# Performance work log

Hardware: AMD Instinct MI355X
Metric: run time of the kernel (lower is better)

The kernel has to match this reference:

```python
import jax, jax.numpy as jnp
import numpy as np

NB_HEAD = 16
SIZE_PER_HEAD = 64
D_MODEL = NB_HEAD * SIZE_PER_HEAD  # 1024
B, S = 4, 2048
NEG_BIG = 1e10


def setup_inputs() -> dict:
    key = jax.random.key(0)
    ks = jax.random.split(key, 9)
    glorot = lambda k, shape: jax.random.uniform(
        k, shape, jnp.float32, -1.0, 1.0) * np.sqrt(6.0 / (shape[0] + shape[1]))
    return {
        "Q_emb": jax.random.normal(ks[0], (B, S, D_MODEL), jnp.float32),
        "K_emb": jax.random.normal(ks[1], (B, S, D_MODEL), jnp.float32),
        "V_emb": jax.random.normal(ks[2], (B, S, D_MODEL), jnp.float32),
        "Q_ini": jax.random.randint(ks[3], (B, S), 0, 50),
        "K_ini": jax.random.randint(ks[4], (B, S), 0, 50),
        "WQ": glorot(ks[5], (D_MODEL, D_MODEL)),
        "WK": glorot(ks[6], (D_MODEL, D_MODEL)),
        "WV": glorot(ks[7], (D_MODEL, D_MODEL)),
        "WO": glorot(ks[8], (D_MODEL, D_MODEL)),
    }


def _proj(x, W):
    # [B,S,D] @ [D, H*dh] -> [B,H,S,dh]
    b, s, _ = x.shape
    y = jnp.einsum('bsd,de->bse', x, W)
    return y.reshape(b, s, NB_HEAD, SIZE_PER_HEAD).transpose(0, 2, 1, 3)


def reference(Q_emb, K_emb, V_emb, Q_ini, K_ini, WQ, WK, WV, WO):
    b, sq, _ = Q_emb.shape
    sk = K_emb.shape[1]
    q = _proj(Q_emb, WQ)
    k = _proj(K_emb, WK)
    v = _proj(V_emb, WV)
    scores = jnp.einsum('bhqd,bhkd->bhqk', q, k) / jnp.sqrt(
        jnp.asarray(SIZE_PER_HEAD, scores_dtype := q.dtype))
    # pad mask: 1 where key token id != 0, broadcast over queries
    pad = (K_ini != 0).astype(scores.dtype)[:, None, None, :]  # [B,1,1,Sk]
    # sub mask: cumsum of eye along rows == lower-triangular causal mask
    causal = jnp.tril(jnp.ones((sq, sk), scores.dtype))[None, None]  # [1,1,Sq,Sk]
    mask = jnp.minimum(pad, causal)
    scores = scores - (1.0 - mask) * NEG_BIG
    attn = jax.nn.softmax(scores, axis=-1)
    ctx = jnp.einsum('bhqk,bhkd->bhqd', attn, v)
    ctx = ctx.transpose(0, 2, 1, 3).reshape(b, sq, NB_HEAD * SIZE_PER_HEAD)
    return jnp.einsum('bsd,de->bse', ctx, WO)
```

## Files before the change

### kernel.cpp

```cpp
#include <hip/hip_runtime.h>

typedef __bf16 bf16_t;
typedef __bf16 bf16x8 __attribute__((ext_vector_type(8)));
typedef __bf16 bf16x4 __attribute__((ext_vector_type(4)));
typedef float  f32x4  __attribute__((ext_vector_type(4)));

#define S_LEN 2048
#define NH    16
#define DH    64
#define DM    1024
#define BATCH 4
#define LOG2E 1.44269504088896f
#define NEGB  (-1.44269504e10f)

static __device__ __forceinline__ f32x4 mfma16(bf16x8 a, bf16x8 b, f32x4 c) {
    return __builtin_amdgcn_mfma_f32_16x16x32_bf16(a, b, c, 0, 0, 0);
}

#if __has_builtin(__builtin_amdgcn_exp2f)
static __device__ __forceinline__ float exp2_hw(float x) {
    return __builtin_amdgcn_exp2f(x);
}
#else
static __device__ __forceinline__ float exp2_hw(float x) {
    float r;
    asm("v_exp_f32 %0, %1" : "=v"(r) : "v"(x));
    return r;
}
#endif

static __device__ __forceinline__ void gl_lds16(const bf16_t* g, bf16_t* l) {
    __builtin_amdgcn_global_load_lds(
        (const __attribute__((address_space(1))) unsigned int*)g,
        (__attribute__((address_space(3))) unsigned int*)l, 16, 0, 0);
}

__global__ __launch_bounds__(256) void cvt3_bf16(const float* __restrict__ s0,
                                                 const float* __restrict__ s1,
                                                 const float* __restrict__ s2,
                                                 bf16_t* __restrict__ d0,
                                                 bf16_t* __restrict__ d1,
                                                 bf16_t* __restrict__ d2, int n) {
    int z = blockIdx.y;
    const float* s = (z == 0) ? s0 : (z == 1) ? s1 : s2;
    bf16_t*      d = (z == 0) ? d0 : (z == 1) ? d1 : d2;
    int i = (blockIdx.x * 256 + threadIdx.x) * 8;
    if (i >= n) return;
    const float4* q = (const float4*)(s + i);
    float4 a = q[0], b = q[1];
    bf16x8 r;
    r[0] = (bf16_t)a.x; r[1] = (bf16_t)a.y; r[2] = (bf16_t)a.z; r[3] = (bf16_t)a.w;
    r[4] = (bf16_t)b.x; r[5] = (bf16_t)b.y; r[6] = (bf16_t)b.z; r[7] = (bf16_t)b.w;
    *(bf16x8*)(d + i) = r;
}

__global__ __launch_bounds__(256) void wtrans(const float* __restrict__ W,
                                              bf16_t* __restrict__ Wt, float scale) {
    __shared__ bf16_t tile[32][33];
    int x = threadIdx.x, ty = threadIdx.y;
    int bx = blockIdx.x * 32, by = blockIdx.y * 32;
#pragma unroll
    for (int i = 0; i < 4; ++i) {
        int y = ty * 4 + i;
        tile[y][x] = (bf16_t)(W[(by + y) * DM + bx + x] * scale);
    }
    __syncthreads();
#pragma unroll
    for (int i = 0; i < 4; ++i) {
        int y = ty * 4 + i;
        Wt[(bx + y) * DM + by + x] = tile[x][y];
    }
}

template <typename CT>
__global__ __launch_bounds__(512) void gemm_nt_256(const bf16_t* __restrict__ A,
                                                   const bf16_t* __restrict__ Bt,
                                                   CT* __restrict__ C,
                                                   int M, int N, int K, float alpha,
                                                   size_t zsA, size_t zsB, size_t zsC,
                                                   int tz, int ldct) {
    __shared__ __align__(16) bf16_t As[2 * 256 * 32];
    __shared__ __align__(16) bf16_t Bs[2 * 128 * 32];
    A  += (size_t)blockIdx.z * zsA;
    Bt += (size_t)blockIdx.z * zsB;
    C  += (size_t)blockIdx.z * zsC;
    int tid = threadIdx.x, wave = tid >> 6, lane = tid & 63;
    int l15 = lane & 15, quad = lane >> 4;
    int wm = wave >> 1, wn = wave & 1;
    int bm = blockIdx.x * 256, bn = blockIdx.y * 128;
    int srow = lane >> 2, skx = (lane & 3) << 3;

    f32x4 acc[4][4] = {};

    for (int k0 = 0; k0 < K; k0 += 64) {
#pragma unroll
        for (int c = 0; c < 4; ++c) {
            int t = wave * 4 + c;
            int kk = t & 1, rb = (t >> 1) * 16;
            gl_lds16(A + (size_t)(bm + rb + srow) * K + k0 + kk * 32 + skx,
                     As + kk * 8192 + rb * 32);
        }
#pragma unroll
        for (int c = 0; c < 2; ++c) {
            int t = wave * 2 + c;
            int kk = t & 1, rb = (t >> 1) * 16;
            gl_lds16(Bt + (size_t)(bn + rb + srow) * K + k0 + kk * 32 + skx,
                     Bs + kk * 4096 + rb * 32);
        }
        __syncthreads();

#pragma unroll
        for (int kk = 0; kk < 2; ++kk) {
            bf16x8 af[4], bfr[4];
#pragma unroll
            for (int i = 0; i < 4; ++i)
                af[i] = *(const bf16x8*)(As + kk * 8192 +
                                         (wm * 64 + i * 16 + l15) * 32 + quad * 8);
#pragma unroll
            for (int j = 0; j < 4; ++j)
                bfr[j] = *(const bf16x8*)(Bs + kk * 4096 +
                                          (wn * 64 + j * 16 + l15) * 32 + quad * 8);
#pragma unroll
            for (int i = 0; i < 4; ++i)
#pragma unroll
                for (int j = 0; j < 4; ++j)
                    acc[i][j] = mfma16(af[i], bfr[j], acc[i][j]);
        }
        __syncthreads();
    }

    if ((int)blockIdx.z == tz) {
#pragma unroll
        for (int i = 0; i < 4; ++i)
#pragma unroll
            for (int j = 0; j < 4; ++j) {
                int n = bn + wn * 64 + j * 16 + l15;
                int m = bm + wm * 64 + i * 16 + quad * 4;
                bf16x4 c;
#pragma unroll
                for (int r = 0; r < 4; ++r) c[r] = (bf16_t)(acc[i][j][r] * alpha);
                *(bf16x4*)((bf16_t*)C + (size_t)n * ldct + m) = c;
            }
    } else {
#pragma unroll
        for (int i = 0; i < 4; ++i)
#pragma unroll
            for (int r = 0; r < 4; ++r) {
                int row = bm + wm * 64 + i * 16 + quad * 4 + r;
#pragma unroll
                for (int j = 0; j < 4; ++j)
                    C[(size_t)row * N + bn + wn * 64 + j * 16 + l15] =
                        (CT)(acc[i][j][r] * alpha);
            }
    }
}

__global__ __launch_bounds__(256) void vmean_vt(const bf16_t* __restrict__ VT,
                                                float* __restrict__ Vm, int ldv) {
    __shared__ float red[64][4];
    int z = blockIdx.y;
    int row = blockIdx.x * 64 + (threadIdx.x >> 2);
    int part = threadIdx.x & 3;
    const bf16_t* p = VT + (size_t)row * ldv + (size_t)z * S_LEN + part * 512;
    float s = 0.f;
    for (int i = 0; i < 64; ++i) {
        bf16x8 v = *(const bf16x8*)(p + i * 8);
#pragma unroll
        for (int j = 0; j < 8; ++j) s += (float)v[j];
    }
    red[threadIdx.x >> 2][part] = s;
    __syncthreads();
    if (threadIdx.x < 64) {
        float t = red[threadIdx.x][0] + red[threadIdx.x][1] +
                  red[threadIdx.x][2] + red[threadIdx.x][3];
        Vm[z * DM + blockIdx.x * 64 + threadIdx.x] = t * (1.0f / S_LEN);
    }
}

__global__ __launch_bounds__(256) void attn_kernel(const bf16_t* __restrict__ Qp,
                                                   const bf16_t* __restrict__ Kp,
                                                   const bf16_t* __restrict__ VT,
                                                   const int* __restrict__ Kini,
                                                   const float* __restrict__ Vmean,
                                                   bf16_t* __restrict__ ctx,
                                                   int ldv, int nqt) {
    __shared__ __align__(16) bf16_t Ks[64 * 72];
    __shared__ __align__(16) bf16_t VsT[64 * 72];
    __shared__ __align__(16) bf16_t Ps[4][16 * 72];
    __shared__ bf16_t padb[2048];

    int bid = blockIdx.x;
    int qt = nqt - 1 - (bid >> 6);
    int hz = bid & 63;
    int h = hz & 15, z = hz >> 4;
    int tid = threadIdx.x, wave = tid >> 6, lane = tid & 63;
    int l15 = lane & 15, quad = lane >> 4;
    int qbase = qt * 64 + wave * 16;
    size_t rowz = (size_t)z * S_LEN;
    int ntiles = qt + 1;
    int nkeys = ntiles * 64;

    for (int i = tid; i < nkeys; i += 256)
        padb[i] = (Kini[rowz + i] == 0) ? (bf16_t)NEGB : (bf16_t)(0.0f);

    const bf16_t* qptr = Qp + (rowz + qbase + l15) * DM + h * DH + quad * 8;
    bf16x8 qa0 = *(const bf16x8*)qptr;
    bf16x8 qa1 = *(const bf16x8*)(qptr + 32);

    f32x4 o[4] = {};
    f32x4 l4 = {0.f, 0.f, 0.f, 0.f};
    int q = qbase + l15;

    int srow = tid >> 2, sch = (tid & 3) << 4;
    const bf16_t* kgb = Kp + (rowz + srow) * DM + h * DH + sch;
    const bf16_t* vgb = VT + (size_t)(h * DH + srow) * ldv + rowz + sch;

    bf16x8 kr0 = *(const bf16x8*)kgb,        kr1 = *(const bf16x8*)(kgb + 8);
    bf16x8 vr0 = *(const bf16x8*)vgb,        vr1 = *(const bf16x8*)(vgb + 8);

    for (int kt = 0; kt < ntiles; ++kt) {
        int kb = kt * 64;
        *(bf16x8*)(Ks  + srow * 72 + sch)     = kr0;
        *(bf16x8*)(Ks  + srow * 72 + sch + 8) = kr1;
        *(bf16x8*)(VsT + srow * 72 + sch)     = vr0;
        *(bf16x8*)(VsT + srow * 72 + sch + 8) = vr1;
        __syncthreads();

        int nkb = (kt + 1 < ntiles) ? kb + 64 : kb;
        const bf16_t* kg = kgb + (size_t)nkb * DM;
        const bf16_t* vg = vgb + nkb;
        kr0 = *(const bf16x8*)kg; kr1 = *(const bf16x8*)(kg + 8);
        vr0 = *(const bf16x8*)vg; vr1 = *(const bf16x8*)(vg + 8);

        f32x4 sv[4];
#pragma unroll
        for (int ks = 0; ks < 4; ++ks) {
            bf16x8 kf0 = *(const bf16x8*)(Ks + (ks * 16 + l15) * 72 + quad * 8);
            bf16x8 kf1 = *(const bf16x8*)(Ks + (ks * 16 + l15) * 72 + 32 + quad * 8);
            f32x4 s = {0.f, 0.f, 0.f, 0.f};
            s = mfma16(kf0, qa0, s);
            s = mfma16(kf1, qa1, s);
            bf16x4 pb = *(const bf16x4*)(padb + kb + ks * 16 + quad * 4);
#pragma unroll
            for (int r = 0; r < 4; ++r) s[r] += (float)pb[r];
            sv[ks] = s;
        }
        if (kt == ntiles - 1) {
#pragma unroll
            for (int ks = 0; ks < 4; ++ks)
#pragma unroll
                for (int r = 0; r < 4; ++r)
                    if (kb + ks * 16 + quad * 4 + r > q) sv[ks][r] = NEGB;
        }

#pragma unroll
        for (int ks = 0; ks < 4; ++ks) {
            f32x4 s = sv[ks];
#pragma unroll
            for (int r = 0; r < 4; ++r) s[r] = exp2_hw(s[r]);
            sv[ks] = s;
        }
        l4 += (sv[0] + sv[1]) + (sv[2] + sv[3]);
#pragma unroll
        for (int ks = 0; ks < 4; ++ks) {
            bf16x4 pk;
#pragma unroll
            for (int r = 0; r < 4; ++r) pk[r] = (bf16_t)sv[ks][r];
            *(bf16x4*)(Ps[wave] + l15 * 72 + ks * 16 + quad * 4) = pk;
        }

        bf16x8 pa0 = *(const bf16x8*)(Ps[wave] + l15 * 72 + quad * 8);
        bf16x8 pa1 = *(const bf16x8*)(Ps[wave] + l15 * 72 + 32 + quad * 8);
#pragma unroll
        for (int j = 0; j < 4; ++j) {
            bf16x8 vb0 = *(const bf16x8*)(VsT + (j * 16 + l15) * 72 + quad * 8);
            bf16x8 vb1 = *(const bf16x8*)(VsT + (j * 16 + l15) * 72 + 32 + quad * 8);
            o[j] = mfma16(vb0, pa0, o[j]);
            o[j] = mfma16(vb1, pa1, o[j]);
        }
        __syncthreads();
    }

    float l_ = (l4[0] + l4[1]) + (l4[2] + l4[3]);
    l_ += __shfl_xor(l_, 16);
    l_ += __shfl_xor(l_, 32);

    float inv = 1.0f / l_;
    bool dead = (l_ == 0.0f);
    if (__any(dead)) {
        const float* vm = Vmean + z * DM + h * DH;
#pragma unroll
        for (int j = 0; j < 4; ++j) {
            bf16x4 c;
#pragma unroll
            for (int r = 0; r < 4; ++r) {
                int dh = j * 16 + quad * 4 + r;
                float val = dead ? vm[dh] : o[j][r] * inv;
                c[r] = (bf16_t)val;
            }
            *(bf16x4*)(Ps[wave] + l15 * 72 + j * 16 + quad * 4) = c;
        }
    } else {
#pragma unroll
        for (int j = 0; j < 4; ++j) {
            bf16x4 c;
#pragma unroll
            for (int r = 0; r < 4; ++r) c[r] = (bf16_t)(o[j][r] * inv);
            *(bf16x4*)(Ps[wave] + l15 * 72 + j * 16 + quad * 4) = c;
        }
    }
    int rr = lane >> 2, cc = (lane & 3) * 16;
    bf16x8 t0 = *(const bf16x8*)(Ps[wave] + rr * 72 + cc);
    bf16x8 t1 = *(const bf16x8*)(Ps[wave] + rr * 72 + cc + 8);
    bf16_t* cp = ctx + (rowz + qbase + rr) * DM + h * DH + cc;
    *(bf16x8*)cp = t0;
    *(bf16x8*)(cp + 8) = t1;
}

extern "C" void kernel_launch(void* const* d_in, const int* in_sizes, int n_in,
                              void* d_out, int out_size, void* d_ws, size_t ws_size,
                              hipStream_t stream) {
    const float* Qe = (const float*)d_in[0];
    const float* Ke = (const float*)d_in[1];
    const float* Ve = (const float*)d_in[2];
    const int* Kini = (const int*)d_in[4];
    const float* WQ = (const float*)d_in[5];
    const float* WK = (const float*)d_in[6];
    const float* WV = (const float*)d_in[7];
    const float* WO = (const float*)d_in[8];
    float* out = (float*)d_out;

    const size_t EMB = (size_t)BATCH * S_LEN * DM;
    const size_t SB  = (size_t)S_LEN * DM;
    const size_t WSZ = (size_t)DM * DM;
    const size_t need_full = (6 * EMB + 4 * WSZ) * sizeof(bf16_t)
                           + (size_t)BATCH * DM * sizeof(float);

    dim3 tb32(32, 8), tg32(32, 32);
    const float qscale = 0.125f * LOG2E;

    if (ws_size >= need_full) {
        bf16_t* Qb  = (bf16_t*)d_ws;
        bf16_t* Kb  = Qb + EMB;
        bf16_t* Vb  = Kb + EMB;
        bf16_t* WQt = Vb + EMB;
        bf16_t* WKt = WQt + WSZ;
        bf16_t* WVt = WKt + WSZ;
        bf16_t* WOt = WVt + WSZ;
        bf16_t* Qp  = WOt + WSZ;
        bf16_t* Kp  = Qp + EMB;
        bf16_t* VT  = Kp + EMB;
        float*  Vm  = (float*)(VT + EMB);
        bf16_t* Cx  = Qp;

        int cg = (int)(EMB / (8 * 256));
        cvt3_bf16<<<dim3(cg, 3), 256, 0, stream>>>(Qe, Ke, Ve, Qb, Kb, Vb, (int)EMB);
        wtrans<<<tg32, tb32, 0, stream>>>(WQ, WQt, qscale);
        wtrans<<<tg32, tb32, 0, stream>>>(WK, WKt, 1.0f);
        wtrans<<<tg32, tb32, 0, stream>>>(WV, WVt, 1.0f);
        wtrans<<<tg32, tb32, 0, stream>>>(WO, WOt, 1.0f);

        gemm_nt_256<bf16_t><<<dim3(8192 / 256, DM / 128, 3), 512, 0, stream>>>(
            Qb, WQt, Qp, 8192, DM, DM, 1.0f, EMB, WSZ, EMB, 2, 8192);

        vmean_vt<<<dim3(DM / 64, BATCH), 256, 0, stream>>>(VT, Vm, 8192);
        attn_kernel<<<dim3((S_LEN / 64) * NH * BATCH), 256, 0, stream>>>(
            Qp, Kp, VT, Kini, Vm, Cx, 8192, S_LEN / 64);

        gemm_nt_256<float><<<dim3(8192 / 256, DM / 128, 1), 512, 0, stream>>>(
            Cx, WOt, out, 8192, DM, DM, 1.0f, 0, 0, 0, -1, 0);
    } else {
        bf16_t* Qb  = (bf16_t*)d_ws;
        bf16_t* Kb  = Qb + SB;
        bf16_t* Vb  = Kb + SB;
        bf16_t* WQt = Vb + SB;
        bf16_t* WKt = WQt + WSZ;
        bf16_t* WVt = WKt + WSZ;
        bf16_t* WOt = WVt + WSZ;
        bf16_t* Qp  = WOt + WSZ;
        bf16_t* Kp  = Qp + SB;
        bf16_t* VT  = Kp + SB;
        float*  Vm  = (float*)(VT + SB);
        bf16_t* Cx  = Qp;

        wtrans<<<tg32, tb32, 0, stream>>>(WQ, WQt, qscale);
        wtrans<<<tg32, tb32, 0, stream>>>(WK, WKt, 1.0f);
        wtrans<<<tg32, tb32, 0, stream>>>(WV, WVt, 1.0f);
        wtrans<<<tg32, tb32, 0, stream>>>(WO, WOt, 1.0f);

        int cg = (int)(SB / (8 * 256));
        for (int b = 0; b < BATCH; ++b) {
            const size_t off = (size_t)b * SB;
            cvt3_bf16<<<dim3(cg, 3), 256, 0, stream>>>(
                Qe + off, Ke + off, Ve + off, Qb, Kb, Vb, (int)SB);
            gemm_nt_256<bf16_t><<<dim3(2048 / 256, DM / 128, 3), 512, 0, stream>>>(
                Qb, WQt, Qp, 2048, DM, DM, 1.0f, SB, WSZ, SB, 2, 2048);
            vmean_vt<<<dim3(DM / 64, 1), 256, 0, stream>>>(VT, Vm, 2048);
            attn_kernel<<<dim3((S_LEN / 64) * NH), 256, 0, stream>>>(
                Qp, Kp, VT, Kini + (size_t)b * S_LEN, Vm, Cx, 2048, S_LEN / 64);
            gemm_nt_256<float><<<dim3(2048 / 256, DM / 128, 1), 512, 0, stream>>>(
                Cx, WOt, out + off, 2048, DM, DM, 1.0f, 0, 0, 0, -1, 0);
        }
    }
}
```

Measured before the change: 342.8 us.

## Double-buffer GEMM LDS tiles with K-step 32 to overlap loads and MFMA

The 256x128 NT GEMM now uses two LDS buffers holding one 32-wide K slice each. The next slice is issued via global-to-LDS loads before the current slice is consumed, so the global loads overlap the MFMA work. This replaces the old scheme, which loaded a 64-wide K slice and then waited at a barrier before computing. The cost is half as much work per iteration and twice as many loop trips. The hidden gl_lds16 wait semantics could also serialize the loads anyway.

```diff
diff --git a/kernel.cpp b/kernel.cpp
--- a/kernel.cpp
+++ b/kernel.cpp
@@ -79,8 +79,8 @@
                                                    int M, int N, int K, float alpha,
                                                    size_t zsA, size_t zsB, size_t zsC,
                                                    int tz, int ldct) {
-    __shared__ __align__(16) bf16_t As[2 * 256 * 32];
-    __shared__ __align__(16) bf16_t Bs[2 * 128 * 32];
+    __shared__ __align__(16) bf16_t As[2][256 * 32];
+    __shared__ __align__(16) bf16_t Bs[2][128 * 32];
     A  += (size_t)blockIdx.z * zsA;
     Bt += (size_t)blockIdx.z * zsB;
     C  += (size_t)blockIdx.z * zsC;
@@ -91,42 +91,38 @@
     int srow = lane >> 2, skx = (lane & 3) << 3;
 
     f32x4 acc[4][4] = {};
-
-    for (int k0 = 0; k0 < K; k0 += 64) {
-#pragma unroll
-        for (int c = 0; c < 4; ++c) {
-            int t = wave * 4 + c;
-            int kk = t & 1, rb = (t >> 1) * 16;
-            gl_lds16(A + (size_t)(bm + rb + srow) * K + k0 + kk * 32 + skx,
-                     As + kk * 8192 + rb * 32);
-        }
+    int nt = K / 32;
+
+    auto STAGE = [&](int b, int k0) {
 #pragma unroll
         for (int c = 0; c < 2; ++c) {
-            int t = wave * 2 + c;
-            int kk = t & 1, rb = (t >> 1) * 16;
-            gl_lds16(Bt + (size_t)(bn + rb + srow) * K + k0 + kk * 32 + skx,
-                     Bs + kk * 4096 + rb * 32);
-        }
+            int s = wave * 2 + c;
+            gl_lds16(A + (size_t)(bm + s * 16 + srow) * K + k0 + skx,
+                     As[b] + s * 512);
+        }
+        gl_lds16(Bt + (size_t)(bn + wave * 16 + srow) * K + k0 + skx,
+                 Bs[b] + wave * 512);
+    };
+
+    STAGE(0, 0);
+    __syncthreads();
+    int cur = 0;
+    for (int t = 0; t < nt; ++t) {
+        if (t + 1 < nt) STAGE(cur ^ 1, (t + 1) * 32);
+        bf16x8 af[4], bfr[4];
+#pragma unroll
+        for (int i = 0; i < 4; ++i)
+            af[i] = *(const bf16x8*)(As[cur] + (wm * 64 + i * 16 + l15) * 32 + quad * 8);
+#pragma unroll
+        for (int j = 0; j < 4; ++j)
+            bfr[j] = *(const bf16x8*)(Bs[cur] + (wn * 64 + j * 16 + l15) * 32 + quad * 8);
+#pragma unroll
+        for (int i = 0; i < 4; ++i)
+#pragma unroll
+            for (int j = 0; j < 4; ++j)
+                acc[i][j] = mfma16(af[i], bfr[j], acc[i][j]);
         __syncthreads();
-
-#pragma unroll
-        for (int kk = 0; kk < 2; ++kk) {
-            bf16x8 af[4], bfr[4];
-#pragma unroll
-            for (int i = 0; i < 4; ++i)
-                af[i] = *(const bf16x8*)(As + kk * 8192 +
-                                         (wm * 64 + i * 16 + l15) * 32 + quad * 8);
-#pragma unroll
-            for (int j = 0; j < 4; ++j)
-                bfr[j] = *(const bf16x8*)(Bs + kk * 4096 +
-                                          (wn * 64 + j * 16 + l15) * 32 + quad * 8);
-#pragma unroll
-            for (int i = 0; i < 4; ++i)
-#pragma unroll
-                for (int j = 0; j < 4; ++j)
-                    acc[i][j] = mfma16(af[i], bfr[j], acc[i][j]);
-        }
-        __syncthreads();
+        cur ^= 1;
     }
 
     if ((int)blockIdx.z == tz) {
```

Measured after the change: 347.1 us. Within noise of the previous version (+1.2%).
